# Kernel optimization log

Measured on AMD Instinct MI355X. Metric: run time of the kernel, lower is better.

Reference implementation:

```python
import jax, jax.numpy as jnp
import numpy as np

B, N, D_IN = 4, 16384, 64          # batch, sequence (grid) length, model dim
H, DH = 8, 64                       # heads, dim per head
INNER = H * DH                      # 512


def setup_inputs() -> dict:
    key = jax.random.key(0)
    ks = jax.random.split(key, 7)
    s = 1.0 / np.sqrt(D_IN)
    return {
        "queries": jax.random.normal(ks[0], (B, N, D_IN), jnp.float32),
        "keys": jax.random.normal(ks[1], (B, N, D_IN), jnp.float32),
        "values": jax.random.normal(ks[2], (B, N, D_IN), jnp.float32),
        # torch nn.Linear weights are [out_features, in_features]
        "Wq": jax.random.normal(ks[3], (INNER, D_IN), jnp.float32) * s,
        "Wk": jax.random.normal(ks[4], (INNER, D_IN), jnp.float32) * s,
        "Wout": jax.random.normal(ks[5], (D_IN, INNER), jnp.float32) * (1.0 / np.sqrt(INNER)),
        "bout": jax.random.normal(ks[6], (D_IN,), jnp.float32) * 0.01,
    }


def reference(queries, keys, values, Wq, Wk, Wout, bout):
    b, n, _ = queries.shape
    # projections (NOTE: source uses to_k for values: values = self.to_k(values))
    q = (queries @ Wq.T).reshape(b, n, H, DH).transpose(0, 2, 1, 3)  # b h n d
    k = (keys    @ Wk.T).reshape(b, n, H, DH).transpose(0, 2, 1, 3)
    v = (values  @ Wk.T).reshape(b, n, H, DH).transpose(0, 2, 1, 3)
    # galerkin linear attention, associative form: (K^T V) first, then Q @ (.)
    # (the instance-norm outputs in the torch source are dead code on this path)
    dots = jnp.einsum('bhnd,bhne->bhde', k, v)            # [b,h,d,d]
    out = jnp.einsum('bhnd,bhde->bhne', q, dots) / n      # [b,h,n,d]
    out = out.transpose(0, 2, 1, 3).reshape(b, n, INNER)  # b n (h d)
    return out @ Wout.T + bout                             # [b,n,D_IN]
```

## Files before the change

kernel.cpp:

```cpp
#include <hip/hip_runtime.h>

#define NB 4
#define SEQ 16384
#define D 64
#define NH 8
#define INNER 512

typedef float f4 __attribute__((ext_vector_type(4)));

#define OFF_S    0
#define OFF_GT   (NB * 4096)
#define OFF_U    (2 * NB * 4096)
#define OFF_PART ((2 * NB + NB * NH) * 4096)

__global__ __launch_bounds__(256) void kA(const float* __restrict__ keys,
                                          const float* __restrict__ values,
                                          float* __restrict__ part) {
    const int bid = blockIdx.x;
    const int b = bid >> 8;
    const int row0 = (bid & 255) * 64;
    const int t = threadIdx.x;
    const int di = t >> 4, ej = t & 15;
    const float* kp = keys   + ((size_t)b * SEQ + row0) * D + di * 4;
    const float* vp = values + ((size_t)b * SEQ + row0) * D + ej * 4;
    f4 acc[4];
    #pragma unroll
    for (int r = 0; r < 4; ++r) acc[r] = (f4)0.f;
    #pragma unroll 8
    for (int n = 0; n < 64; ++n) {
        f4 k4 = *(const f4*)(kp + n * D);
        f4 v4 = *(const f4*)(vp + n * D);
        #pragma unroll
        for (int r = 0; r < 4; ++r)
            acc[r] += k4[r] * v4;
    }
    float* pp = part + (size_t)bid * 4096;
    #pragma unroll
    for (int r = 0; r < 4; ++r)
        *(f4*)(pp + (di * 4 + r) * 64 + ej * 4) = acc[r];
}

__global__ __launch_bounds__(256) void kB(const float* __restrict__ part,
                                          float* __restrict__ S) {
    const int bid = blockIdx.x;
    const int b  = bid >> 5;
    const int q  = (bid >> 3) & 3;
    const int pc = bid & 7;
    const int t = threadIdx.x;
    const int e0 = q * 1024 + t * 4;
    const float* pp = part + (size_t)(b * 256 + pc * 32) * 4096 + e0;
    f4 s = (f4)0.f;
    #pragma unroll 8
    for (int p = 0; p < 32; ++p)
        s += *(const f4*)(pp + (size_t)p * 4096);
    float* Sb = S + b * 4096 + e0;
    #pragma unroll
    for (int i = 0; i < 4; ++i)
        atomicAdd(&Sb[i], s[i]);
}

__global__ __launch_bounds__(256) void kC1(const float* __restrict__ Wk,
                                           float* __restrict__ ws) {
    __shared__ float T[64 * 65];
    const int b = blockIdx.x >> 3, h = blockIdx.x & 7;
    const int t = threadIdx.x;
    const int di = t >> 4, ej = t & 15;
    const float* Sb  = ws + OFF_S + b * 4096;
    const float* Wkh = Wk + (size_t)h * 64 * D;

    f4 acc[4];
    #pragma unroll
    for (int r = 0; r < 4; ++r) acc[r] = (f4)0.f;
    for (int j4 = 0; j4 < 16; ++j4) {
        f4 ak[4], bs[4];
        #pragma unroll
        for (int r = 0; r < 4; ++r)  ak[r] = *(const f4*)(Wkh + (di * 4 + r) * D + j4 * 4);
        #pragma unroll
        for (int jj = 0; jj < 4; ++jj) bs[jj] = *(const f4*)(Sb + (j4 * 4 + jj) * D + ej * 4);
        #pragma unroll
        for (int r = 0; r < 4; ++r)
            #pragma unroll
            for (int jj = 0; jj < 4; ++jj)
                acc[r] += ak[r][jj] * bs[jj];
    }
    #pragma unroll
    for (int r = 0; r < 4; ++r)
        #pragma unroll
        for (int c = 0; c < 4; ++c)
            T[(di * 4 + r) * 65 + ej * 4 + ((c + di) & 3)] = acc[r][c];
    __syncthreads();

    float a2[4][4];
    #pragma unroll
    for (int r = 0; r < 4; ++r)
        #pragma unroll
        for (int c = 0; c < 4; ++c) a2[r][c] = 0.f;
    for (int i4 = 0; i4 < 16; ++i4) {
        float av[4][4];
        f4 bw[4];
        #pragma unroll
        for (int ii = 0; ii < 4; ++ii)
            #pragma unroll
            for (int r = 0; r < 4; ++r)
                av[r][ii] = T[(di * 4 + r) * 65 + i4 * 4 + ((ii + di) & 3)];
        #pragma unroll
        for (int c = 0; c < 4; ++c)
            bw[c] = *(const f4*)(Wkh + (ej * 4 + c) * D + i4 * 4);
        #pragma unroll
        for (int r = 0; r < 4; ++r)
            #pragma unroll
            for (int c = 0; c < 4; ++c)
                #pragma unroll
                for (int ii = 0; ii < 4; ++ii)
                    a2[r][c] = fmaf(av[r][ii], bw[c][ii], a2[r][c]);
    }
    float* Up = ws + OFF_U + (size_t)(b * 8 + h) * 4096;
    #pragma unroll
    for (int r = 0; r < 4; ++r) {
        f4 o; o[0] = a2[r][0]; o[1] = a2[r][1]; o[2] = a2[r][2]; o[3] = a2[r][3];
        *(f4*)(Up + (di * 4 + r) * 64 + ej * 4) = o;
    }
}

__global__ __launch_bounds__(256) void kC2(const float* __restrict__ Wq,
                                           const float* __restrict__ Wout,
                                           float* __restrict__ ws) {
    __shared__ float T[64 * 65];
    const int b = blockIdx.x >> 3, h = blockIdx.x & 7;
    const int t = threadIdx.x;
    const int di = t >> 4, ej = t & 15;
    const float* Up = ws + OFF_U + (size_t)(b * 8 + h) * 4096;

    float acc[4][4];
    #pragma unroll
    for (int r = 0; r < 4; ++r)
        #pragma unroll
        for (int c = 0; c < 4; ++c) acc[r][c] = 0.f;
    for (int i4 = 0; i4 < 16; ++i4) {
        f4 wq4[4], bu[4];
        #pragma unroll
        for (int ii = 0; ii < 4; ++ii) {
            wq4[ii] = *(const f4*)(Wq + (size_t)(64 * h + i4 * 4 + ii) * D + di * 4);
            bu[ii]  = *(const f4*)(Up + (i4 * 4 + ii) * 64 + ej * 4);
        }
        #pragma unroll
        for (int r = 0; r < 4; ++r)
            #pragma unroll
            for (int c = 0; c < 4; ++c)
                #pragma unroll
                for (int ii = 0; ii < 4; ++ii)
                    acc[r][c] = fmaf(wq4[ii][r], bu[ii][c], acc[r][c]);
    }
    #pragma unroll
    for (int r = 0; r < 4; ++r)
        #pragma unroll
        for (int c = 0; c < 4; ++c)
            T[(di * 4 + r) * 65 + ej * 4 + ((c + di) & 3)] = acc[r][c];
    __syncthreads();

    float a2[4][4];
    #pragma unroll
    for (int r = 0; r < 4; ++r)
        #pragma unroll
        for (int c = 0; c < 4; ++c) a2[r][c] = 0.f;
    for (int i4 = 0; i4 < 16; ++i4) {
        float av[4][4];
        f4 bw[4];
        #pragma unroll
        for (int ii = 0; ii < 4; ++ii)
            #pragma unroll
            for (int r = 0; r < 4; ++r)
                av[r][ii] = T[(di * 4 + r) * 65 + i4 * 4 + ((ii + di) & 3)];
        #pragma unroll
        for (int c = 0; c < 4; ++c)
            bw[c] = *(const f4*)(Wout + (size_t)(ej * 4 + c) * INNER + 64 * h + i4 * 4);
        #pragma unroll
        for (int r = 0; r < 4; ++r)
            #pragma unroll
            for (int c = 0; c < 4; ++c)
                #pragma unroll
                for (int ii = 0; ii < 4; ++ii)
                    a2[r][c] = fmaf(av[r][ii], bw[c][ii], a2[r][c]);
    }
    const float invn = 1.0f / (float)SEQ;
    float* GTb = ws + OFF_GT + b * 4096;
    #pragma unroll
    for (int r = 0; r < 4; ++r)
        #pragma unroll
        for (int c = 0; c < 4; ++c)
            atomicAdd(&GTb[(ej * 4 + c) * 64 + di * 4 + r], a2[r][c] * invn);
}

__global__ __launch_bounds__(256) void kE(const float* __restrict__ queries,
                                          const float* __restrict__ bout,
                                          const float* __restrict__ ws,
                                          float* __restrict__ out) {
    const int bid = blockIdx.x;
    const int b = bid >> 8;
    const int row0 = (bid & 255) * 64;
    const int t = threadIdx.x;
    const int w = t >> 6, l = t & 63;
    const int rg = l >> 4, eg = l & 15;
    const float* GT = ws + OFF_GT + b * 4096;
    const size_t rbase = (size_t)b * SEQ + row0 + w * 16 + rg * 4;
    const float* qp = queries + rbase * D;
    float acc[4][4];
    #pragma unroll
    for (int r = 0; r < 4; ++r)
        #pragma unroll
        for (int c = 0; c < 4; ++c) acc[r][c] = 0.f;
    #pragma unroll 2
    for (int dq = 0; dq < 16; ++dq) {
        f4 q4[4], g4[4];
        #pragma unroll
        for (int r = 0; r < 4; ++r)
            q4[r] = *(const f4*)(qp + r * D + dq * 4);
        #pragma unroll
        for (int c = 0; c < 4; ++c)
            g4[c] = *(const f4*)(GT + (eg * 4 + c) * 64 + dq * 4);
        #pragma unroll
        for (int r = 0; r < 4; ++r)
            #pragma unroll
            for (int c = 0; c < 4; ++c)
                #pragma unroll
                for (int ii = 0; ii < 4; ++ii)
                    acc[r][c] = fmaf(q4[r][ii], g4[c][ii], acc[r][c]);
    }
    const f4 bo = *(const f4*)(bout + eg * 4);
    float* op = out + rbase * D;
    #pragma unroll
    for (int r = 0; r < 4; ++r) {
        f4 o;
        o[0] = acc[r][0] + bo[0]; o[1] = acc[r][1] + bo[1];
        o[2] = acc[r][2] + bo[2]; o[3] = acc[r][3] + bo[3];
        *(f4*)(op + r * D + eg * 4) = o;
    }
}

extern "C" void kernel_launch(void* const* d_in, const int* in_sizes, int n_in,
                              void* d_out, int out_size, void* d_ws, size_t ws_size,
                              hipStream_t stream) {
    const float* queries = (const float*)d_in[0];
    const float* keys    = (const float*)d_in[1];
    const float* values  = (const float*)d_in[2];
    const float* Wq      = (const float*)d_in[3];
    const float* Wk      = (const float*)d_in[4];
    const float* Wout    = (const float*)d_in[5];
    const float* bout    = (const float*)d_in[6];
    float* ws = (float*)d_ws;

    hipMemsetAsync(ws, 0, (size_t)2 * NB * 4096 * sizeof(float), stream);

    kA <<<1024, 256, 0, stream>>>(keys, values, ws + OFF_PART);
    kB <<<128,  256, 0, stream>>>(ws + OFF_PART, ws + OFF_S);
    kC1<<<32,   256, 0, stream>>>(Wk, ws);
    kC2<<<32,   256, 0, stream>>>(Wq, Wout, ws);
    kE <<<1024, 256, 0, stream>>>(queries, bout, ws, (float*)d_out);
}
```

Baseline: 184.3 us.

## Fuse weight-side kernels and halve per-block rows in reduction and output kernels

Merges the two small 32-block kernels kC1 and kC2 into one kernel that keeps the intermediate U matrix in shared memory, removing one launch and a global round trip through the workspace. The partial-sum kernel kA and the output kernel kE now process 32 rows per block with 2048 blocks, so each kernel exposes more parallelism across the GPU. kB is adjusted to reduce the doubled number of partials. The cost is more partial-sum traffic and a larger partial buffer, plus smaller per-thread work in kE.

```diff
diff --git a/kernel.cpp b/kernel.cpp
--- a/kernel.cpp
+++ b/kernel.cpp
@@ -10,15 +10,14 @@
 
 #define OFF_S    0
 #define OFF_GT   (NB * 4096)
-#define OFF_U    (2 * NB * 4096)
-#define OFF_PART ((2 * NB + NB * NH) * 4096)
+#define OFF_PART (2 * NB * 4096)
 
 __global__ __launch_bounds__(256) void kA(const float* __restrict__ keys,
                                           const float* __restrict__ values,
                                           float* __restrict__ part) {
     const int bid = blockIdx.x;
-    const int b = bid >> 8;
-    const int row0 = (bid & 255) * 64;
+    const int b = bid >> 9;
+    const int row0 = (bid & 511) * 32;
     const int t = threadIdx.x;
     const int di = t >> 4, ej = t & 15;
     const float* kp = keys   + ((size_t)b * SEQ + row0) * D + di * 4;
@@ -27,7 +26,7 @@
     #pragma unroll
     for (int r = 0; r < 4; ++r) acc[r] = (f4)0.f;
     #pragma unroll 8
-    for (int n = 0; n < 64; ++n) {
+    for (int n = 0; n < 32; ++n) {
         f4 k4 = *(const f4*)(kp + n * D);
         f4 v4 = *(const f4*)(vp + n * D);
         #pragma unroll
@@ -43,12 +42,12 @@
 __global__ __launch_bounds__(256) void kB(const float* __restrict__ part,
                                           float* __restrict__ S) {
     const int bid = blockIdx.x;
-    const int b  = bid >> 5;
-    const int q  = (bid >> 3) & 3;
-    const int pc = bid & 7;
+    const int b  = bid >> 6;
+    const int q  = (bid >> 4) & 3;
+    const int pc = bid & 15;
     const int t = threadIdx.x;
     const int e0 = q * 1024 + t * 4;
-    const float* pp = part + (size_t)(b * 256 + pc * 32) * 4096 + e0;
+    const float* pp = part + (size_t)(b * 512 + pc * 32) * 4096 + e0;
     f4 s = (f4)0.f;
     #pragma unroll 8
     for (int p = 0; p < 32; ++p)
@@ -59,136 +58,141 @@
         atomicAdd(&Sb[i], s[i]);
 }
 
-__global__ __launch_bounds__(256) void kC1(const float* __restrict__ Wk,
-                                           float* __restrict__ ws) {
+__global__ __launch_bounds__(256) void kC(const float* __restrict__ Wq,
+                                          const float* __restrict__ Wk,
+                                          const float* __restrict__ Wout,
+                                          float* __restrict__ ws) {
     __shared__ float T[64 * 65];
+    __shared__ float U[64 * 65];
     const int b = blockIdx.x >> 3, h = blockIdx.x & 7;
     const int t = threadIdx.x;
     const int di = t >> 4, ej = t & 15;
     const float* Sb  = ws + OFF_S + b * 4096;
     const float* Wkh = Wk + (size_t)h * 64 * D;
 
-    f4 acc[4];
-    #pragma unroll
-    for (int r = 0; r < 4; ++r) acc[r] = (f4)0.f;
-    for (int j4 = 0; j4 < 16; ++j4) {
-        f4 ak[4], bs[4];
-        #pragma unroll
-        for (int r = 0; r < 4; ++r)  ak[r] = *(const f4*)(Wkh + (di * 4 + r) * D + j4 * 4);
-        #pragma unroll
-        for (int jj = 0; jj < 4; ++jj) bs[jj] = *(const f4*)(Sb + (j4 * 4 + jj) * D + ej * 4);
-        #pragma unroll
-        for (int r = 0; r < 4; ++r)
-            #pragma unroll
-            for (int jj = 0; jj < 4; ++jj)
-                acc[r] += ak[r][jj] * bs[jj];
-    }
-    #pragma unroll
-    for (int r = 0; r < 4; ++r)
-        #pragma unroll
-        for (int c = 0; c < 4; ++c)
-            T[(di * 4 + r) * 65 + ej * 4 + ((c + di) & 3)] = acc[r][c];
+    {
+        f4 acc[4];
+        #pragma unroll
+        for (int r = 0; r < 4; ++r) acc[r] = (f4)0.f;
+        for (int j4 = 0; j4 < 16; ++j4) {
+            f4 ak[4], bs[4];
+            #pragma unroll
+            for (int r = 0; r < 4; ++r)  ak[r] = *(const f4*)(Wkh + (di * 4 + r) * D + j4 * 4);
+            #pragma unroll
+            for (int jj = 0; jj < 4; ++jj) bs[jj] = *(const f4*)(Sb + (j4 * 4 + jj) * D + ej * 4);
+            #pragma unroll
+            for (int r = 0; r < 4; ++r)
+                #pragma unroll
+                for (int jj = 0; jj < 4; ++jj)
+                    acc[r] += ak[r][jj] * bs[jj];
+        }
+        #pragma unroll
+        for (int r = 0; r < 4; ++r)
+            #pragma unroll
+            for (int c = 0; c < 4; ++c)
+                T[(di * 4 + r) * 65 + ej * 4 + ((c + di) & 3)] = acc[r][c];
+    }
     __syncthreads();
 
-    float a2[4][4];
-    #pragma unroll
-    for (int r = 0; r < 4; ++r)
-        #pragma unroll
-        for (int c = 0; c < 4; ++c) a2[r][c] = 0.f;
-    for (int i4 = 0; i4 < 16; ++i4) {
-        float av[4][4];
-        f4 bw[4];
-        #pragma unroll
-        for (int ii = 0; ii < 4; ++ii)
-            #pragma unroll
-            for (int r = 0; r < 4; ++r)
-                av[r][ii] = T[(di * 4 + r) * 65 + i4 * 4 + ((ii + di) & 3)];
-        #pragma unroll
-        for (int c = 0; c < 4; ++c)
-            bw[c] = *(const f4*)(Wkh + (ej * 4 + c) * D + i4 * 4);
-        #pragma unroll
-        for (int r = 0; r < 4; ++r)
-            #pragma unroll
-            for (int c = 0; c < 4; ++c)
-                #pragma unroll
-                for (int ii = 0; ii < 4; ++ii)
-                    a2[r][c] = fmaf(av[r][ii], bw[c][ii], a2[r][c]);
-    }
-    float* Up = ws + OFF_U + (size_t)(b * 8 + h) * 4096;
-    #pragma unroll
-    for (int r = 0; r < 4; ++r) {
-        f4 o; o[0] = a2[r][0]; o[1] = a2[r][1]; o[2] = a2[r][2]; o[3] = a2[r][3];
-        *(f4*)(Up + (di * 4 + r) * 64 + ej * 4) = o;
-    }
-}
-
-__global__ __launch_bounds__(256) void kC2(const float* __restrict__ Wq,
-                                           const float* __restrict__ Wout,
-                                           float* __restrict__ ws) {
-    __shared__ float T[64 * 65];
-    const int b = blockIdx.x >> 3, h = blockIdx.x & 7;
-    const int t = threadIdx.x;
-    const int di = t >> 4, ej = t & 15;
-    const float* Up = ws + OFF_U + (size_t)(b * 8 + h) * 4096;
-
-    float acc[4][4];
-    #pragma unroll
-    for (int r = 0; r < 4; ++r)
-        #pragma unroll
-        for (int c = 0; c < 4; ++c) acc[r][c] = 0.f;
-    for (int i4 = 0; i4 < 16; ++i4) {
-        f4 wq4[4], bu[4];
-        #pragma unroll
-        for (int ii = 0; ii < 4; ++ii) {
-            wq4[ii] = *(const f4*)(Wq + (size_t)(64 * h + i4 * 4 + ii) * D + di * 4);
-            bu[ii]  = *(const f4*)(Up + (i4 * 4 + ii) * 64 + ej * 4);
-        }
-        #pragma unroll
-        for (int r = 0; r < 4; ++r)
-            #pragma unroll
-            for (int c = 0; c < 4; ++c)
-                #pragma unroll
-                for (int ii = 0; ii < 4; ++ii)
-                    acc[r][c] = fmaf(wq4[ii][r], bu[ii][c], acc[r][c]);
-    }
-    #pragma unroll
-    for (int r = 0; r < 4; ++r)
-        #pragma unroll
-        for (int c = 0; c < 4; ++c)
-            T[(di * 4 + r) * 65 + ej * 4 + ((c + di) & 3)] = acc[r][c];
+    {
+        float a2[4][4];
+        #pragma unroll
+        for (int r = 0; r < 4; ++r)
+            #pragma unroll
+            for (int c = 0; c < 4; ++c) a2[r][c] = 0.f;
+        for (int i4 = 0; i4 < 16; ++i4) {
+            float av[4][4];
+            f4 bw[4];
+            #pragma unroll
+            for (int ii = 0; ii < 4; ++ii)
+                #pragma unroll
+                for (int r = 0; r < 4; ++r)
+                    av[r][ii] = T[(di * 4 + r) * 65 + i4 * 4 + ((ii + di) & 3)];
+            #pragma unroll
+            for (int c = 0; c < 4; ++c)
+                bw[c] = *(const f4*)(Wkh + (ej * 4 + c) * D + i4 * 4);
+            #pragma unroll
+            for (int r = 0; r < 4; ++r)
+                #pragma unroll
+                for (int c = 0; c < 4; ++c)
+                    #pragma unroll
+                    for (int ii = 0; ii < 4; ++ii)
+                        a2[r][c] = fmaf(av[r][ii], bw[c][ii], a2[r][c]);
+        }
+        #pragma unroll
+        for (int r = 0; r < 4; ++r)
+            #pragma unroll
+            for (int c = 0; c < 4; ++c)
+                U[(di * 4 + r) * 65 + ej * 4 + ((c + di) & 3)] = a2[r][c];
+    }
     __syncthreads();
 
-    float a2[4][4];
-    #pragma unroll
-    for (int r = 0; r < 4; ++r)
-        #pragma unroll
-        for (int c = 0; c < 4; ++c) a2[r][c] = 0.f;
-    for (int i4 = 0; i4 < 16; ++i4) {
-        float av[4][4];
-        f4 bw[4];
-        #pragma unroll
-        for (int ii = 0; ii < 4; ++ii)
-            #pragma unroll
-            for (int r = 0; r < 4; ++r)
-                av[r][ii] = T[(di * 4 + r) * 65 + i4 * 4 + ((ii + di) & 3)];
-        #pragma unroll
-        for (int c = 0; c < 4; ++c)
-            bw[c] = *(const f4*)(Wout + (size_t)(ej * 4 + c) * INNER + 64 * h + i4 * 4);
-        #pragma unroll
-        for (int r = 0; r < 4; ++r)
-            #pragma unroll
-            for (int c = 0; c < 4; ++c)
-                #pragma unroll
-                for (int ii = 0; ii < 4; ++ii)
-                    a2[r][c] = fmaf(av[r][ii], bw[c][ii], a2[r][c]);
-    }
-    const float invn = 1.0f / (float)SEQ;
-    float* GTb = ws + OFF_GT + b * 4096;
-    #pragma unroll
-    for (int r = 0; r < 4; ++r)
-        #pragma unroll
-        for (int c = 0; c < 4; ++c)
-            atomicAdd(&GTb[(ej * 4 + c) * 64 + di * 4 + r], a2[r][c] * invn);
+    {
+        float acc[4][4];
+        #pragma unroll
+        for (int r = 0; r < 4; ++r)
+            #pragma unroll
+            for (int c = 0; c < 4; ++c) acc[r][c] = 0.f;
+        for (int i4 = 0; i4 < 16; ++i4) {
+            f4 wq4[4];
+            float bu[4][4];
+            #pragma unroll
+            for (int ii = 0; ii < 4; ++ii) {
+                wq4[ii] = *(const f4*)(Wq + (size_t)(64 * h + i4 * 4 + ii) * D + di * 4);
+                #pragma unroll
+                for (int c = 0; c < 4; ++c)
+                    bu[ii][c] = U[(i4 * 4 + ii) * 65 + ej * 4 + ((c + i4) & 3)];
+            }
+            #pragma unroll
+            for (int r = 0; r < 4; ++r)
+                #pragma unroll
+                for (int c = 0; c < 4; ++c)
+                    #pragma unroll
+                    for (int ii = 0; ii < 4; ++ii)
+                        acc[r][c] = fmaf(wq4[ii][r], bu[ii][c], acc[r][c]);
+        }
+        __syncthreads();
+        #pragma unroll
+        for (int r = 0; r < 4; ++r)
+            #pragma unroll
+            for (int c = 0; c < 4; ++c)
+                T[(di * 4 + r) * 65 + ej * 4 + ((c + di) & 3)] = acc[r][c];
+    }
+    __syncthreads();
+
+    {
+        float a2[4][4];
+        #pragma unroll
+        for (int r = 0; r < 4; ++r)
+            #pragma unroll
+            for (int c = 0; c < 4; ++c) a2[r][c] = 0.f;
+        for (int i4 = 0; i4 < 16; ++i4) {
+            float av[4][4];
+            f4 bw[4];
+            #pragma unroll
+            for (int ii = 0; ii < 4; ++ii)
+                #pragma unroll
+                for (int r = 0; r < 4; ++r)
+                    av[r][ii] = T[(di * 4 + r) * 65 + i4 * 4 + ((ii + di) & 3)];
+            #pragma unroll
+            for (int c = 0; c < 4; ++c)
+                bw[c] = *(const f4*)(Wout + (size_t)(ej * 4 + c) * INNER + 64 * h + i4 * 4);
+            #pragma unroll
+            for (int r = 0; r < 4; ++r)
+                #pragma unroll
+                for (int c = 0; c < 4; ++c)
+                    #pragma unroll
+                    for (int ii = 0; ii < 4; ++ii)
+                        a2[r][c] = fmaf(av[r][ii], bw[c][ii], a2[r][c]);
+        }
+        const float invn = 1.0f / (float)SEQ;
+        float* GTb = ws + OFF_GT + b * 4096;
+        #pragma unroll
+        for (int r = 0; r < 4; ++r)
+            #pragma unroll
+            for (int c = 0; c < 4; ++c)
+                atomicAdd(&GTb[(ej * 4 + c) * 64 + di * 4 + r], a2[r][c] * invn);
+    }
 }
 
 __global__ __launch_bounds__(256) void kE(const float* __restrict__ queries,
@@ -196,40 +200,39 @@
                                           const float* __restrict__ ws,
                                           float* __restrict__ out) {
     const int bid = blockIdx.x;
-    const int b = bid >> 8;
-    const int row0 = (bid & 255) * 64;
-    const int t = threadIdx.x;
-    const int w = t >> 6, l = t & 63;
-    const int rg = l >> 4, eg = l & 15;
+    const int b = bid >> 9;
+    const int row0 = (bid & 511) * 32;
+    const int t = threadIdx.x;
+    const int rg = t >> 4;
+    const int eg = t & 15;
     const float* GT = ws + OFF_GT + b * 4096;
-    const size_t rbase = (size_t)b * SEQ + row0 + w * 16 + rg * 4;
+    const size_t rbase = (size_t)b * SEQ + row0 + rg * 2;
     const float* qp = queries + rbase * D;
-    float acc[4][4];
-    #pragma unroll
-    for (int r = 0; r < 4; ++r)
+    float acc[2][4];
+    #pragma unroll
+    for (int r = 0; r < 2; ++r)
         #pragma unroll
         for (int c = 0; c < 4; ++c) acc[r][c] = 0.f;
-    #pragma unroll 2
+    #pragma unroll 4
     for (int dq = 0; dq < 16; ++dq) {
-        f4 q4[4], g4[4];
-        #pragma unroll
-        for (int r = 0; r < 4; ++r)
-            q4[r] = *(const f4*)(qp + r * D + dq * 4);
+        f4 q0 = *(const f4*)(qp + dq * 4);
+        f4 q1 = *(const f4*)(qp + D + dq * 4);
+        f4 g4[4];
         #pragma unroll
         for (int c = 0; c < 4; ++c)
             g4[c] = *(const f4*)(GT + (eg * 4 + c) * 64 + dq * 4);
         #pragma unroll
-        for (int r = 0; r < 4; ++r)
-            #pragma unroll
-            for (int c = 0; c < 4; ++c)
-                #pragma unroll
-                for (int ii = 0; ii < 4; ++ii)
-                    acc[r][c] = fmaf(q4[r][ii], g4[c][ii], acc[r][c]);
+        for (int c = 0; c < 4; ++c)
+            #pragma unroll
+            for (int ii = 0; ii < 4; ++ii) {
+                acc[0][c] = fmaf(q0[ii], g4[c][ii], acc[0][c]);
+                acc[1][c] = fmaf(q1[ii], g4[c][ii], acc[1][c]);
+            }
     }
     const f4 bo = *(const f4*)(bout + eg * 4);
     float* op = out + rbase * D;
     #pragma unroll
-    for (int r = 0; r < 4; ++r) {
+    for (int r = 0; r < 2; ++r) {
         f4 o;
         o[0] = acc[r][0] + bo[0]; o[1] = acc[r][1] + bo[1];
         o[2] = acc[r][2] + bo[2]; o[3] = acc[r][3] + bo[3];
@@ -251,9 +254,8 @@
 
     hipMemsetAsync(ws, 0, (size_t)2 * NB * 4096 * sizeof(float), stream);
 
-    kA <<<1024, 256, 0, stream>>>(keys, values, ws + OFF_PART);
-    kB <<<128,  256, 0, stream>>>(ws + OFF_PART, ws + OFF_S);
-    kC1<<<32,   256, 0, stream>>>(Wk, ws);
-    kC2<<<32,   256, 0, stream>>>(Wq, Wout, ws);
-    kE <<<1024, 256, 0, stream>>>(queries, bout, ws, (float*)d_out);
-}
+    kA<<<2048, 256, 0, stream>>>(keys, values, ws + OFF_PART);
+    kB<<<256,  256, 0, stream>>>(ws + OFF_PART, ws + OFF_S);
+    kC<<<32,   256, 0, stream>>>(Wq, Wk, Wout, ws);
+    kE<<<2048, 256, 0, stream>>>(queries, bout, ws, (float*)d_out);
+}
```

New measurement: 215.6 us. +17.0%, slower.
